# Performance work log

Hardware: AMD Instinct MI355X
Metric: run time of the kernel (lower is better)

The kernel has to match this reference:

```python
import jax, jax.numpy as jnp
import numpy as np

N, E, D, L, G = 100000, 800000, 64, 5, 256
ATOM_VOCAB, BOND_VOCAB = 119, 5
BN_EPS = 1e-5

def _bn(h, g, b):
    # BatchNorm1d in training mode: batch mean / biased var over nodes
    m = h.mean(0)
    v = h.var(0)
    return g * (h - m) * jax.lax.rsqrt(v + BN_EPS) + b

def setup_inputs() -> dict:
    key = jax.random.key(0)
    ks = jax.random.split(key, 12)
    xavier = lambda k, fi, fo: jax.random.uniform(k, (fi, fo), jnp.float32,
                                                  -np.sqrt(6.0/(fi+fo)), np.sqrt(6.0/(fi+fo)))
    return {
        "batch": jnp.sort(jax.random.randint(ks[0], (N,), 0, G)),
        "x": jax.random.randint(ks[1], (N, 1), 0, ATOM_VOCAB),
        "edge_index": jax.random.randint(ks[2], (2, E), 0, N),
        "edge_attr": jax.random.randint(ks[3], (E, 1), 0, BOND_VOCAB),
        "atom_emb": jax.random.normal(ks[4], (ATOM_VOCAB, D), jnp.float32),
        "bond_emb": jax.random.normal(ks[5], (BOND_VOCAB, D), jnp.float32),
        "W1": jnp.stack([xavier(jax.random.fold_in(ks[6], i), D, 2*D) for i in range(L)]),
        "b1": jnp.zeros((L, 2*D), jnp.float32),
        "g1": jnp.ones((L, 2*D), jnp.float32),
        "be1": jnp.zeros((L, 2*D), jnp.float32),
        "W2": jnp.stack([xavier(jax.random.fold_in(ks[7], i), 2*D, D) for i in range(L)]),
        "b2": jnp.zeros((L, D), jnp.float32),
        "gbn": jnp.ones((L, D), jnp.float32),
        "bbn": jnp.zeros((L, D), jnp.float32),
    }

def reference(batch, x, edge_index, edge_attr, atom_emb, bond_emb,
              W1, b1, g1, be1, W2, b2, gbn, bbn):
    h = atom_emb[x[:, 0]]              # [N, D]
    ea = bond_emb[edge_attr[:, 0]]     # [E, D]
    src, dst = edge_index[0], edge_index[1]
    for i in range(L):
        msg = jax.nn.relu(h[src] + ea)                         # [E, D]
        aggr = jax.ops.segment_sum(msg, dst, num_segments=N)   # [N, D]
        z = h + aggr                                           # (1+eps)*x_i + aggr, eps=0
        z = _bn(z @ W1[i] + b1[i], g1[i], be1[i])
        z = jax.nn.relu(z) @ W2[i] + b2[i]
        h = _bn(z, gbn[i], bbn[i])                             # outer BN
        if i < L - 1:
            h = jax.nn.relu(h)                                 # drop_ratio = 0 -> no dropout
    xpool = jax.ops.segment_sum(h, batch, num_segments=G)      # global_add_pool
    return (xpool, h)
```

## Files before the change

### kernel.cpp

```cpp
#include <hip/hip_runtime.h>
#include <cstdint>
#include <cstddef>

#define NN 100000
#define NP 100032
#define NE 800000
#define NG 256
#define NL 5
#define EPS 1e-5f

typedef __bf16 bf16x8 __attribute__((ext_vector_type(8)));
typedef float f32x4 __attribute__((ext_vector_type(4)));

__device__ __forceinline__ float bf2f(unsigned short u) {
  union { unsigned int i; float f; } x; x.i = ((unsigned int)u) << 16; return x.f;
}
__device__ __forceinline__ unsigned short f2bf(float f) {
  union { float f; unsigned int i; } x; x.f = f;
  unsigned int r = x.i + 0x7fffu + ((x.i >> 16) & 1u);
  return (unsigned short)(r >> 16);
}

__global__ __launch_bounds__(256) void init_h_k(const int* __restrict__ x,
                                                const float* __restrict__ atom_emb,
                                                unsigned short* __restrict__ A) {
  int i = blockIdx.x * 256 + threadIdx.x;
  int n = i >> 3, c0 = (i & 7) * 8;
  const float* p = atom_emb + (size_t)x[n] * 64 + c0;
  float4 v0 = *(const float4*)p;
  float4 v1 = *(const float4*)(p + 4);
  union { bf16x8 b; unsigned short u[8]; } o;
  o.u[0] = f2bf(v0.x); o.u[1] = f2bf(v0.y); o.u[2] = f2bf(v0.z); o.u[3] = f2bf(v0.w);
  o.u[4] = f2bf(v1.x); o.u[5] = f2bf(v1.y); o.u[6] = f2bf(v1.z); o.u[7] = f2bf(v1.w);
  *(bf16x8*)(A + (size_t)n * 64 + c0) = o.b;
}

__global__ __launch_bounds__(256) void wconv_k(const float* __restrict__ W1,
                                               const float* __restrict__ W2,
                                               unsigned short* __restrict__ Wt1,
                                               unsigned short* __restrict__ Wt2) {
  int i = blockIdx.x * 256 + threadIdx.x;
  const int S = NL * 128 * 64;
  if (i < S) {
    int l = i / (128 * 64), r = i % (128 * 64);
    int c = r / 64, k = r % 64;
    Wt1[i] = f2bf(W1[(size_t)l * 64 * 128 + (size_t)k * 128 + c]);
  } else if (i < 2 * S) {
    int j = i - S;
    int l = j / (128 * 64), r = j % (128 * 64);
    int c = r / 128, k = r % 128;
    Wt2[j] = f2bf(W2[(size_t)l * 128 * 64 + (size_t)k * 64 + c]);
  }
}

__global__ __launch_bounds__(256) void hist_k(const int* __restrict__ ei,
                                              int* __restrict__ cnt) {
  int e = blockIdx.x * 256 + threadIdx.x;
  if (e >= NE) return;
  atomicAdd(&cnt[ei[NE + e]], 1);
}

__global__ __launch_bounds__(256) void scan1_k(const int* __restrict__ cnt,
                                               int* __restrict__ rs,
                                               int* __restrict__ bsum) {
  __shared__ int sh[256];
  int t = threadIdx.x;
  int base = blockIdx.x * 1024 + t * 4;
  int v0 = 0, v1 = 0, v2 = 0, v3 = 0;
  if (base + 0 < NN) v0 = cnt[base + 0];
  if (base + 1 < NN) v1 = cnt[base + 1];
  if (base + 2 < NN) v2 = cnt[base + 2];
  if (base + 3 < NN) v3 = cnt[base + 3];
  int tsum = v0 + v1 + v2 + v3;
  sh[t] = tsum;
  __syncthreads();
  for (int off = 1; off < 256; off <<= 1) {
    int x = (t >= off) ? sh[t - off] : 0;
    __syncthreads();
    sh[t] += x;
    __syncthreads();
  }
  int excl = sh[t] - tsum;
  if (base + 0 < NN) rs[base + 0] = excl;
  if (base + 1 < NN) rs[base + 1] = excl + v0;
  if (base + 2 < NN) rs[base + 2] = excl + v0 + v1;
  if (base + 3 < NN) rs[base + 3] = excl + v0 + v1 + v2;
  if (t == 255) bsum[blockIdx.x] = sh[255];
}

__global__ void scan2_k(const int* __restrict__ bsum, int* __restrict__ bofs, int nb) {
  if (threadIdx.x == 0 && blockIdx.x == 0) {
    int run = 0;
    for (int i = 0; i < nb; ++i) { bofs[i] = run; run += bsum[i]; }
  }
}

__global__ __launch_bounds__(256) void scan3_k(int* __restrict__ rs,
                                               const int* __restrict__ bofs,
                                               int* __restrict__ cursor) {
  int i = blockIdx.x * 256 + threadIdx.x;
  if (i < NN) {
    int v = rs[i] + bofs[i >> 10];
    rs[i] = v;
    cursor[i] = v;
  }
  if (i == 0) rs[NN] = NE;
}

__global__ __launch_bounds__(256) void scatter_k(const int* __restrict__ ei,
                                                 const int* __restrict__ eattr,
                                                 int* __restrict__ cursor,
                                                 int* __restrict__ epack) {
  int band = blockIdx.x & 7;
  int e = (blockIdx.x >> 3) * 256 + threadIdx.x;
  if (e >= NE) return;
  int d = ei[NE + e];
  if (d / 12500 != band) return;
  int slot = atomicAdd(&cursor[d], 1);
  epack[slot] = (ei[e] << 3) | eattr[e];
}

template <int MODE>
__global__ __launch_bounds__(256) void csr_aggr_k(const int* __restrict__ rowstart,
                                                  const int* __restrict__ epack,
                                                  const float* __restrict__ bond,
                                                  const unsigned short* __restrict__ A,
                                                  const float* __restrict__ stat2prev,
                                                  const float* __restrict__ g,
                                                  const float* __restrict__ be,
                                                  unsigned short* __restrict__ B) {
  __shared__ float bl[5][68];
  __shared__ float scl64[64], shf64[64];
  int tid = threadIdx.x;
  for (int j = tid; j < 320; j += 256) bl[j >> 6][j & 63] = bond[j];
  if (MODE && tid < 64) {
    float s = 0.f, s2 = 0.f;
#pragma unroll
    for (int r = 0; r < 8; ++r) { s += stat2prev[r * 128 + tid]; s2 += stat2prev[r * 128 + 64 + tid]; }
    float mean = s * (1.f / NN);
    float var = fmaxf(s2 * (1.f / NN) - mean * mean, 0.f);
    float sc = g[tid] * rsqrtf(var + EPS);
    scl64[tid] = sc;
    shf64[tid] = be[tid] - mean * sc;
  }
  __syncthreads();

  int w = tid >> 6, lane = tid & 63;
  int es = lane >> 3, cg = lane & 7, c0 = cg * 8;
  float sc[8], sf[8];
  if (MODE) {
#pragma unroll
    for (int j = 0; j < 8; ++j) { sc[j] = scl64[c0 + j]; sf[j] = shf64[c0 + j]; }
  }
  int base16 = blockIdx.x * 16 + w * 4;
#pragma unroll
  for (int r4 = 0; r4 < 4; ++r4) {
    int w0 = base16 + r4;
    int s = rowstart[w0], e = rowstart[w0 + 1];
    float acc[8];
#pragma unroll
    for (int j = 0; j < 8; ++j) acc[j] = 0.f;
    for (int base = s; base < e; base += 64) {
      int m = e - base; if (m > 64) m = 64;
      int pk = (lane < m) ? epack[base + lane] : 0;
      int iters = (m + 7) >> 3;
      for (int i = 0; i < iters; ++i) {
        int idx = i * 8 + es;
        int p = __shfl(pk, idx);
        if (idx < m) {
          union { bf16x8 b; unsigned short u[8]; } hv;
          hv.b = *(const bf16x8*)(A + (size_t)(p >> 3) * 64 + c0);
          const float* bp = &bl[p & 7][c0];
          float4 b0 = *(const float4*)(bp);
          float4 b1 = *(const float4*)(bp + 4);
          float bb[8] = {b0.x, b0.y, b0.z, b0.w, b1.x, b1.y, b1.z, b1.w};
#pragma unroll
          for (int j = 0; j < 8; ++j) {
            float v = bf2f(hv.u[j]);
            if (MODE) v = fmaxf(fmaf(v, sc[j], sf[j]), 0.f);
            acc[j] += fmaxf(v + bb[j], 0.f);
          }
        }
      }
    }
#pragma unroll
    for (int j = 0; j < 8; ++j) {
      acc[j] += __shfl_xor(acc[j], 8);
      acc[j] += __shfl_xor(acc[j], 16);
      acc[j] += __shfl_xor(acc[j], 32);
    }
    if (es == 0) {
      union { bf16x8 b; unsigned short u[8]; } rv, o;
      rv.b = *(const bf16x8*)(A + (size_t)w0 * 64 + c0);
#pragma unroll
      for (int j = 0; j < 8; ++j) {
        float r = bf2f(rv.u[j]);
        if (MODE) r = fmaxf(fmaf(r, sc[j], sf[j]), 0.f);
        o.u[j] = f2bf(acc[j] + r);
      }
      *(bf16x8*)(B + (size_t)w0 * 64 + c0) = o.b;
    }
  }
}

__global__ __launch_bounds__(256) void stat1_k(const unsigned short* __restrict__ B,
                                               const unsigned short* __restrict__ Wt1,
                                               float* __restrict__ stat1) {
  int tid = threadIdx.x;
  int w = tid >> 6, lane = tid & 63;
  int rlo = lane & 15, khi = lane >> 4;
  bf16x8 wf0[8], wf1[8];
#pragma unroll
  for (int ct = 0; ct < 8; ++ct) {
    const bf16x8* bp = (const bf16x8*)(Wt1 + (size_t)(ct * 16 + rlo) * 64 + khi * 8);
    wf0[ct] = bp[0];
    wf1[ct] = bp[4];
  }
  float s[8], s2[8];
#pragma unroll
  for (int ct = 0; ct < 8; ++ct) { s[ct] = 0.f; s2[ct] = 0.f; }
  union { bf16x8 b; uint4 u; } zz; zz.u = make_uint4(0, 0, 0, 0);
  for (int t = blockIdx.x * 4 + w; t < NP / 16; t += 1024) {
    int row = t * 16 + rlo;
    bf16x8 a0, a1;
    if (row < NN) {
      const bf16x8* ap = (const bf16x8*)(B + (size_t)row * 64 + khi * 8);
      a0 = ap[0]; a1 = ap[4];
    } else {
      a0 = zz.b; a1 = zz.b;
    }
#pragma unroll
    for (int ct = 0; ct < 8; ++ct) {
      f32x4 acc;
      acc[0] = 0.f; acc[1] = 0.f; acc[2] = 0.f; acc[3] = 0.f;
      acc = __builtin_amdgcn_mfma_f32_16x16x32_bf16(a0, wf0[ct], acc, 0, 0, 0);
      acc = __builtin_amdgcn_mfma_f32_16x16x32_bf16(a1, wf1[ct], acc, 0, 0, 0);
#pragma unroll
      for (int q = 0; q < 4; ++q) {
        s[ct] += acc[q];
        s2[ct] = fmaf(acc[q], acc[q], s2[ct]);
      }
    }
  }
#pragma unroll
  for (int ct = 0; ct < 8; ++ct) {
    s[ct] += __shfl_xor(s[ct], 16);  s[ct] += __shfl_xor(s[ct], 32);
    s2[ct] += __shfl_xor(s2[ct], 16); s2[ct] += __shfl_xor(s2[ct], 32);
  }
  if (khi == 0) {
    float* dst = stat1 + (blockIdx.x & 7) * 256;
#pragma unroll
    for (int ct = 0; ct < 8; ++ct) {
      atomicAdd(&dst[ct * 16 + rlo], s[ct]);
      atomicAdd(&dst[128 + ct * 16 + rlo], s2[ct]);
    }
  }
}

__global__ __launch_bounds__(256) void gemm12_k(const unsigned short* __restrict__ B,
                                                const unsigned short* __restrict__ Wt1,
                                                const unsigned short* __restrict__ Wt2,
                                                const float* __restrict__ stat1,
                                                const float* __restrict__ g1,
                                                const float* __restrict__ be1,
                                                const float* __restrict__ b2,
                                                unsigned short* __restrict__ z2b,
                                                float* __restrict__ stat2f) {
  __shared__ unsigned short Zs[64][136];
  __shared__ float sclS[128], shfS[128], sred[128];
  int tid = threadIdx.x;
  if (tid < 128) {
    float s = 0.f, s2 = 0.f;
#pragma unroll
    for (int r = 0; r < 8; ++r) { s += stat1[r * 256 + tid]; s2 += stat1[r * 256 + 128 + tid]; }
    float mean = s * (1.f / NN);
    float var = fmaxf(s2 * (1.f / NN) - mean * mean, 0.f);
    float sc = g1[tid] * rsqrtf(var + EPS);
    sclS[tid] = sc;
    shfS[tid] = be1[tid] - mean * sc;
    sred[tid] = 0.f;
  }
  __syncthreads();
  int w = tid >> 6, lane = tid & 63;
  int rlo = lane & 15, khi = lane >> 4;
  int row0 = blockIdx.x * 64 + w * 16;
  const bf16x8* ap = (const bf16x8*)(B + (size_t)(row0 + rlo) * 64 + khi * 8);
  bf16x8 a0 = ap[0], a1 = ap[4];
#pragma unroll
  for (int ct = 0; ct < 8; ++ct) {
    const bf16x8* bp = (const bf16x8*)(Wt1 + (size_t)(ct * 16 + rlo) * 64 + khi * 8);
    f32x4 acc;
    acc[0] = 0.f; acc[1] = 0.f; acc[2] = 0.f; acc[3] = 0.f;
    acc = __builtin_amdgcn_mfma_f32_16x16x32_bf16(a0, bp[0], acc, 0, 0, 0);
    acc = __builtin_amdgcn_mfma_f32_16x16x32_bf16(a1, bp[4], acc, 0, 0, 0);
    int c = ct * 16 + rlo;
    float sc = sclS[c], sf = shfS[c];
#pragma unroll
    for (int q = 0; q < 4; ++q)
      Zs[w * 16 + khi * 4 + q][c] = f2bf(fmaxf(fmaf(acc[q], sc, sf), 0.f));
  }
  bf16x8 af0 = *(const bf16x8*)&Zs[w * 16 + rlo][khi * 8];
  bf16x8 af1 = *(const bf16x8*)&Zs[w * 16 + rlo][32 + khi * 8];
  bf16x8 af2 = *(const bf16x8*)&Zs[w * 16 + rlo][64 + khi * 8];
  bf16x8 af3 = *(const bf16x8*)&Zs[w * 16 + rlo][96 + khi * 8];
  __syncthreads();
  f32x4 acc2[4];
#pragma unroll
  for (int ct = 0; ct < 4; ++ct) { acc2[ct][0] = 0.f; acc2[ct][1] = 0.f; acc2[ct][2] = 0.f; acc2[ct][3] = 0.f; }
#pragma unroll
  for (int ct = 0; ct < 4; ++ct) {
    const bf16x8* bp = (const bf16x8*)(Wt2 + (size_t)(ct * 16 + rlo) * 128 + khi * 8);
    acc2[ct] = __builtin_amdgcn_mfma_f32_16x16x32_bf16(af0, bp[0], acc2[ct], 0, 0, 0);
    acc2[ct] = __builtin_amdgcn_mfma_f32_16x16x32_bf16(af1, bp[4], acc2[ct], 0, 0, 0);
    acc2[ct] = __builtin_amdgcn_mfma_f32_16x16x32_bf16(af2, bp[8], acc2[ct], 0, 0, 0);
    acc2[ct] = __builtin_amdgcn_mfma_f32_16x16x32_bf16(af3, bp[12], acc2[ct], 0, 0, 0);
  }
  unsigned short (*Z2)[72] = (unsigned short(*)[72])Zs;
#pragma unroll
  for (int ct = 0; ct < 4; ++ct) {
    int c = ct * 16 + rlo;
    float bs = b2[c];
    float s = 0.f, s2 = 0.f;
#pragma unroll
    for (int q = 0; q < 4; ++q) {
      int brow = w * 16 + khi * 4 + q;
      float v = acc2[ct][q] + bs;
      unsigned short ub = f2bf(v);
      Z2[brow][c] = ub;
      float vf = bf2f(ub);
      if (blockIdx.x * 64 + brow < NN) { s += vf; s2 += vf * vf; }
    }
    atomicAdd(&sred[c], s);
    atomicAdd(&sred[64 + c], s2);
  }
  __syncthreads();
#pragma unroll
  for (int pass = 0; pass < 2; ++pass) {
    int orow = pass * 32 + (tid >> 3), oc0 = (tid & 7) * 8;
    *(bf16x8*)(z2b + (size_t)(blockIdx.x * 64 + orow) * 64 + oc0) =
        *(const bf16x8*)&Z2[orow][oc0];
  }
  if (tid < 128) atomicAdd(&stat2f[(blockIdx.x & 7) * 128 + tid], sred[tid]);
}

__global__ __launch_bounds__(256) void bn_final_k(const unsigned short* __restrict__ A,
                                                  const float* __restrict__ stat2f,
                                                  const float* __restrict__ g,
                                                  const float* __restrict__ be,
                                                  float* __restrict__ hf) {
  __shared__ float scl[64], shf[64];
  int tid = threadIdx.x;
  if (tid < 64) {
    float s = 0.f, s2 = 0.f;
#pragma unroll
    for (int r = 0; r < 8; ++r) { s += stat2f[r * 128 + tid]; s2 += stat2f[r * 128 + 64 + tid]; }
    float mean = s * (1.f / NN);
    float var = fmaxf(s2 * (1.f / NN) - mean * mean, 0.f);
    float sc = g[tid] * rsqrtf(var + EPS);
    scl[tid] = sc;
    shf[tid] = be[tid] - mean * sc;
  }
  __syncthreads();
  int i = blockIdx.x * 256 + tid;
  int n = i >> 3, c0 = (i & 7) * 8;
  union { bf16x8 b; unsigned short u[8]; } raw;
  raw.b = *(const bf16x8*)(A + (size_t)n * 64 + c0);
  float v[8];
#pragma unroll
  for (int j = 0; j < 8; ++j) v[j] = fmaf(bf2f(raw.u[j]), scl[c0 + j], shf[c0 + j]);
  float* p = hf + (size_t)n * 64 + c0;
  *(float4*)(p)     = make_float4(v[0], v[1], v[2], v[3]);
  *(float4*)(p + 4) = make_float4(v[4], v[5], v[6], v[7]);
}

__global__ __launch_bounds__(256) void pool_k(const float* __restrict__ h,
                                              const int* __restrict__ batch,
                                              float* __restrict__ xpool) {
  int n0 = blockIdx.x * 16;
  int tid = threadIdx.x;
  int r = tid >> 4, c4 = tid & 15;
  int n = n0 + r;
  float4 v = *(const float4*)(h + (size_t)n * 64 + c4 * 4);
  __shared__ int gfirst, gsame;
  __shared__ float red[16][64];
  if (tid == 0) {
    gfirst = batch[n0];
    gsame = (batch[n0] == batch[n0 + 15]) ? 1 : 0;
  }
  *(float4*)&red[r][c4 * 4] = v;
  __syncthreads();
  if (gsame) {
#pragma unroll
    for (int off = 8; off >= 1; off >>= 1) {
      if (r < off) {
        float4 a = *(float4*)&red[r][c4 * 4];
        float4 b = *(float4*)&red[r + off][c4 * 4];
        *(float4*)&red[r][c4 * 4] = make_float4(a.x + b.x, a.y + b.y, a.z + b.z, a.w + b.w);
      }
      __syncthreads();
    }
    if (r == 0) {
      float* p = xpool + (size_t)gfirst * 64 + c4 * 4;
      float4 a = *(float4*)&red[0][c4 * 4];
      atomicAdd(p + 0, a.x); atomicAdd(p + 1, a.y);
      atomicAdd(p + 2, a.z); atomicAdd(p + 3, a.w);
    }
  } else {
    int g = batch[n];
    float* p = xpool + (size_t)g * 64 + c4 * 4;
    atomicAdd(p + 0, v.x); atomicAdd(p + 1, v.y);
    atomicAdd(p + 2, v.z); atomicAdd(p + 3, v.w);
  }
}

extern "C" void kernel_launch(void* const* d_in, const int* in_sizes, int n_in,
                              void* d_out, int out_size, void* d_ws, size_t ws_size,
                              hipStream_t stream) {
  const int* batch = (const int*)d_in[0];
  const int* x = (const int*)d_in[1];
  const int* ei = (const int*)d_in[2];
  const int* eattr = (const int*)d_in[3];
  const float* atom_emb = (const float*)d_in[4];
  const float* bond_emb = (const float*)d_in[5];
  const float* W1 = (const float*)d_in[6];
  const float* g1 = (const float*)d_in[8];
  const float* be1 = (const float*)d_in[9];
  const float* W2 = (const float*)d_in[10];
  const float* b2 = (const float*)d_in[11];
  const float* gbn = (const float*)d_in[12];
  const float* bbn = (const float*)d_in[13];

  float* out = (float*)d_out;
  float* xpool = out;
  float* hf = out + NG * 64;

  char* ws = (char*)d_ws;
  unsigned short* A   = (unsigned short*)(ws);
  unsigned short* B   = (unsigned short*)(ws + 12804096);
  float* sbuf         = (float*)(ws + 25608192);
  unsigned short* Wt1 = (unsigned short*)(ws + 25669632);
  unsigned short* Wt2 = (unsigned short*)(ws + 25751552);
  int* rowstart       = (int*)(ws + 25833472);
  int* epack          = (int*)(ws + 26233600);
  int* cnt    = (int*)(ws + 12804096);
  int* cursor = (int*)(ws + 12804096 + 1048576);
  int* bsum   = (int*)(ws + 12804096 + 2097152);
  int* bofs   = bsum + 128;

  init_h_k<<<NN * 8 / 256, 256, 0, stream>>>(x, atom_emb, A);
  wconv_k<<<(2 * NL * 128 * 64 + 255) / 256, 256, 0, stream>>>(W1, W2, Wt1, Wt2);

  hipMemsetAsync(cnt, 0, (size_t)NN * 4, stream);
  hist_k<<<(NE + 255) / 256, 256, 0, stream>>>(ei, cnt);
  scan1_k<<<98, 256, 0, stream>>>(cnt, rowstart, bsum);
  scan2_k<<<1, 64, 0, stream>>>(bsum, bofs, 98);
  scan3_k<<<(NN + 255) / 256, 256, 0, stream>>>(rowstart, bofs, cursor);
  scatter_k<<<8 * ((NE + 255) / 256), 256, 0, stream>>>(ei, eattr, cursor, epack);

  hipMemsetAsync(sbuf, 0, 61440, stream);
  for (int l = 0; l < NL; ++l) {
    float* stat1 = sbuf + (size_t)l * 3072;
    float* stat2 = sbuf + (size_t)l * 3072 + 2048;
    float* stat2p = sbuf + (size_t)(l - 1) * 3072 + 2048;
    if (l == 0)
      csr_aggr_k<0><<<NN / 16, 256, 0, stream>>>(rowstart, epack, bond_emb, A,
                                                 sbuf, gbn, bbn, B);
    else
      csr_aggr_k<1><<<NN / 16, 256, 0, stream>>>(rowstart, epack, bond_emb, A,
                                                 stat2p, gbn + (size_t)(l - 1) * 64,
                                                 bbn + (size_t)(l - 1) * 64, B);
    stat1_k<<<256, 256, 0, stream>>>(B, Wt1 + (size_t)l * 128 * 64, stat1);
    gemm12_k<<<NP / 64, 256, 0, stream>>>(B, Wt1 + (size_t)l * 128 * 64,
                                          Wt2 + (size_t)l * 64 * 128,
                                          stat1, g1 + (size_t)l * 128, be1 + (size_t)l * 128,
                                          b2 + (size_t)l * 64, A, stat2);
  }

  bn_final_k<<<NN * 8 / 256, 256, 0, stream>>>(A, sbuf + (size_t)(NL - 1) * 3072 + 2048,
                                               gbn + (size_t)(NL - 1) * 64,
                                               bbn + (size_t)(NL - 1) * 64, hf);

  hipMemsetAsync(xpool, 0, (size_t)NG * 64 * 4, stream);
  pool_k<<<NN / 16, 256, 0, stream>>>(hf, batch, xpool);
}
```

Baseline: 600.4 us.

## Merge prep kernels, fold scan2 into scan3, remap CSR aggregation, fuse BN with pooling

Merges the embedding init, the weight conversion and the count zeroing into a single prep kernel. The serial scan2 kernel is dropped, and each scan3 block now sums the block totals it needs itself. The CSR aggregation kernel now gives each 8-lane group one destination row, unrolled two edges at a time, instead of spreading a row's edges across the whole wavefront and reducing with shuffles. The final BN and global add pool are fused so the output is not re-read. Together these aim to cut launch count and memory traffic, but per-row work in aggregation now depends on node degree, which can leave lanes idle.

Measured after the change: 506.6 us. 1.19x faster.

```diff
diff --git a/kernel.cpp b/kernel.cpp
--- a/kernel.cpp
+++ b/kernel.cpp
@@ -21,35 +21,41 @@
   return (unsigned short)(r >> 16);
 }
 
-__global__ __launch_bounds__(256) void init_h_k(const int* __restrict__ x,
-                                                const float* __restrict__ atom_emb,
-                                                unsigned short* __restrict__ A) {
-  int i = blockIdx.x * 256 + threadIdx.x;
-  int n = i >> 3, c0 = (i & 7) * 8;
-  const float* p = atom_emb + (size_t)x[n] * 64 + c0;
-  float4 v0 = *(const float4*)p;
-  float4 v1 = *(const float4*)(p + 4);
-  union { bf16x8 b; unsigned short u[8]; } o;
-  o.u[0] = f2bf(v0.x); o.u[1] = f2bf(v0.y); o.u[2] = f2bf(v0.z); o.u[3] = f2bf(v0.w);
-  o.u[4] = f2bf(v1.x); o.u[5] = f2bf(v1.y); o.u[6] = f2bf(v1.z); o.u[7] = f2bf(v1.w);
-  *(bf16x8*)(A + (size_t)n * 64 + c0) = o.b;
-}
-
-__global__ __launch_bounds__(256) void wconv_k(const float* __restrict__ W1,
-                                               const float* __restrict__ W2,
-                                               unsigned short* __restrict__ Wt1,
-                                               unsigned short* __restrict__ Wt2) {
-  int i = blockIdx.x * 256 + threadIdx.x;
-  const int S = NL * 128 * 64;
-  if (i < S) {
-    int l = i / (128 * 64), r = i % (128 * 64);
-    int c = r / 64, k = r % 64;
-    Wt1[i] = f2bf(W1[(size_t)l * 64 * 128 + (size_t)k * 128 + c]);
-  } else if (i < 2 * S) {
-    int j = i - S;
-    int l = j / (128 * 64), r = j % (128 * 64);
-    int c = r / 128, k = r % 128;
-    Wt2[j] = f2bf(W2[(size_t)l * 128 * 64 + (size_t)k * 64 + c]);
+__global__ __launch_bounds__(256) void prep_k(const int* __restrict__ x,
+                                              const float* __restrict__ atom_emb,
+                                              unsigned short* __restrict__ A,
+                                              const float* __restrict__ W1,
+                                              const float* __restrict__ W2,
+                                              unsigned short* __restrict__ Wt1,
+                                              unsigned short* __restrict__ Wt2,
+                                              int* __restrict__ cnt) {
+  int b = blockIdx.x, t = threadIdx.x;
+  if (b < 3125) {
+    int i = b * 256 + t;
+    int n = i >> 3, c0 = (i & 7) * 8;
+    const float* p = atom_emb + (size_t)x[n] * 64 + c0;
+    float4 v0 = *(const float4*)p;
+    float4 v1 = *(const float4*)(p + 4);
+    union { bf16x8 b8; unsigned short u[8]; } o;
+    o.u[0] = f2bf(v0.x); o.u[1] = f2bf(v0.y); o.u[2] = f2bf(v0.z); o.u[3] = f2bf(v0.w);
+    o.u[4] = f2bf(v1.x); o.u[5] = f2bf(v1.y); o.u[6] = f2bf(v1.z); o.u[7] = f2bf(v1.w);
+    *(bf16x8*)(A + (size_t)n * 64 + c0) = o.b8;
+  } else if (b < 3445) {
+    int i = (b - 3125) * 256 + t;
+    const int S = NL * 128 * 64;
+    if (i < S) {
+      int l = i / (128 * 64), r = i % (128 * 64);
+      int c = r / 64, k = r % 64;
+      Wt1[i] = f2bf(W1[(size_t)l * 64 * 128 + (size_t)k * 128 + c]);
+    } else {
+      int j = i - S;
+      int l = j / (128 * 64), r = j % (128 * 64);
+      int c = r / 128, k = r % 128;
+      Wt2[j] = f2bf(W2[(size_t)l * 128 * 64 + (size_t)k * 64 + c]);
+    }
+  } else {
+    int i = (b - 3445) * 256 + t;
+    if (i < NN) cnt[i] = 0;
   }
 }
 
@@ -88,19 +94,15 @@
   if (t == 255) bsum[blockIdx.x] = sh[255];
 }
 
-__global__ void scan2_k(const int* __restrict__ bsum, int* __restrict__ bofs, int nb) {
-  if (threadIdx.x == 0 && blockIdx.x == 0) {
-    int run = 0;
-    for (int i = 0; i < nb; ++i) { bofs[i] = run; run += bsum[i]; }
-  }
-}
-
 __global__ __launch_bounds__(256) void scan3_k(int* __restrict__ rs,
-                                               const int* __restrict__ bofs,
+                                               const int* __restrict__ bsum,
                                                int* __restrict__ cursor) {
   int i = blockIdx.x * 256 + threadIdx.x;
+  int chunk = blockIdx.x >> 2;
+  int boff = 0;
+  for (int j = 0; j < chunk; ++j) boff += bsum[j];
   if (i < NN) {
-    int v = rs[i] + bofs[i >> 10];
+    int v = rs[i] + boff;
     rs[i] = v;
     cursor[i] = v;
   }
@@ -145,62 +147,65 @@
   }
   __syncthreads();
 
-  int w = tid >> 6, lane = tid & 63;
-  int es = lane >> 3, cg = lane & 7, c0 = cg * 8;
+  int lane = tid & 63;
+  int sg = lane >> 3, ch = lane & 7, c0 = ch * 8;
+  int row = blockIdx.x * 32 + (tid >> 6) * 8 + sg;
   float sc[8], sf[8];
   if (MODE) {
 #pragma unroll
     for (int j = 0; j < 8; ++j) { sc[j] = scl64[c0 + j]; sf[j] = shf64[c0 + j]; }
   }
-  int base16 = blockIdx.x * 16 + w * 4;
-#pragma unroll
-  for (int r4 = 0; r4 < 4; ++r4) {
-    int w0 = base16 + r4;
-    int s = rowstart[w0], e = rowstart[w0 + 1];
-    float acc[8];
-#pragma unroll
-    for (int j = 0; j < 8; ++j) acc[j] = 0.f;
-    for (int base = s; base < e; base += 64) {
-      int m = e - base; if (m > 64) m = 64;
-      int pk = (lane < m) ? epack[base + lane] : 0;
-      int iters = (m + 7) >> 3;
-      for (int i = 0; i < iters; ++i) {
-        int idx = i * 8 + es;
-        int p = __shfl(pk, idx);
-        if (idx < m) {
-          union { bf16x8 b; unsigned short u[8]; } hv;
-          hv.b = *(const bf16x8*)(A + (size_t)(p >> 3) * 64 + c0);
-          const float* bp = &bl[p & 7][c0];
-          float4 b0 = *(const float4*)(bp);
-          float4 b1 = *(const float4*)(bp + 4);
-          float bb[8] = {b0.x, b0.y, b0.z, b0.w, b1.x, b1.y, b1.z, b1.w};
-#pragma unroll
-          for (int j = 0; j < 8; ++j) {
-            float v = bf2f(hv.u[j]);
-            if (MODE) v = fmaxf(fmaf(v, sc[j], sf[j]), 0.f);
-            acc[j] += fmaxf(v + bb[j], 0.f);
-          }
-        }
+  int s = rowstart[row], e = rowstart[row + 1];
+  float acc[8];
+#pragma unroll
+  for (int j = 0; j < 8; ++j) acc[j] = 0.f;
+  int i = s;
+  for (; i + 2 <= e; i += 2) {
+    int p0 = epack[i], p1 = epack[i + 1];
+    union { bf16x8 b; unsigned short u[8]; } h0, h1;
+    h0.b = *(const bf16x8*)(A + (size_t)(p0 >> 3) * 64 + c0);
+    h1.b = *(const bf16x8*)(A + (size_t)(p1 >> 3) * 64 + c0);
+    const float* bp0 = &bl[p0 & 7][c0];
+    const float* bp1 = &bl[p1 & 7][c0];
+    float4 a0 = *(const float4*)(bp0), a1 = *(const float4*)(bp0 + 4);
+    float4 d0 = *(const float4*)(bp1), d1 = *(const float4*)(bp1 + 4);
+    float bb0[8] = {a0.x, a0.y, a0.z, a0.w, a1.x, a1.y, a1.z, a1.w};
+    float bb1[8] = {d0.x, d0.y, d0.z, d0.w, d1.x, d1.y, d1.z, d1.w};
+#pragma unroll
+    for (int j = 0; j < 8; ++j) {
+      float v0 = bf2f(h0.u[j]);
+      float v1 = bf2f(h1.u[j]);
+      if (MODE) {
+        v0 = fmaxf(fmaf(v0, sc[j], sf[j]), 0.f);
+        v1 = fmaxf(fmaf(v1, sc[j], sf[j]), 0.f);
       }
-    }
+      acc[j] += fmaxf(v0 + bb0[j], 0.f);
+      acc[j] += fmaxf(v1 + bb1[j], 0.f);
+    }
+  }
+  if (i < e) {
+    int p0 = epack[i];
+    union { bf16x8 b; unsigned short u[8]; } h0;
+    h0.b = *(const bf16x8*)(A + (size_t)(p0 >> 3) * 64 + c0);
+    const float* bp0 = &bl[p0 & 7][c0];
+    float4 a0 = *(const float4*)(bp0), a1 = *(const float4*)(bp0 + 4);
+    float bb0[8] = {a0.x, a0.y, a0.z, a0.w, a1.x, a1.y, a1.z, a1.w};
 #pragma unroll
     for (int j = 0; j < 8; ++j) {
-      acc[j] += __shfl_xor(acc[j], 8);
-      acc[j] += __shfl_xor(acc[j], 16);
-      acc[j] += __shfl_xor(acc[j], 32);
-    }
-    if (es == 0) {
-      union { bf16x8 b; unsigned short u[8]; } rv, o;
-      rv.b = *(const bf16x8*)(A + (size_t)w0 * 64 + c0);
-#pragma unroll
-      for (int j = 0; j < 8; ++j) {
-        float r = bf2f(rv.u[j]);
-        if (MODE) r = fmaxf(fmaf(r, sc[j], sf[j]), 0.f);
-        o.u[j] = f2bf(acc[j] + r);
-      }
-      *(bf16x8*)(B + (size_t)w0 * 64 + c0) = o.b;
-    }
-  }
+      float v0 = bf2f(h0.u[j]);
+      if (MODE) v0 = fmaxf(fmaf(v0, sc[j], sf[j]), 0.f);
+      acc[j] += fmaxf(v0 + bb0[j], 0.f);
+    }
+  }
+  union { bf16x8 b; unsigned short u[8]; } rv, o;
+  rv.b = *(const bf16x8*)(A + (size_t)row * 64 + c0);
+#pragma unroll
+  for (int j = 0; j < 8; ++j) {
+    float r = bf2f(rv.u[j]);
+    if (MODE) r = fmaxf(fmaf(r, sc[j], sf[j]), 0.f);
+    o.u[j] = f2bf(acc[j] + r);
+  }
+  *(bf16x8*)(B + (size_t)row * 64 + c0) = o.b;
 }
 
 __global__ __launch_bounds__(256) void stat1_k(const unsigned short* __restrict__ B,
@@ -343,12 +348,16 @@
   if (tid < 128) atomicAdd(&stat2f[(blockIdx.x & 7) * 128 + tid], sred[tid]);
 }
 
-__global__ __launch_bounds__(256) void bn_final_k(const unsigned short* __restrict__ A,
-                                                  const float* __restrict__ stat2f,
-                                                  const float* __restrict__ g,
-                                                  const float* __restrict__ be,
-                                                  float* __restrict__ hf) {
+__global__ __launch_bounds__(256) void final_k(const unsigned short* __restrict__ A,
+                                               const float* __restrict__ stat2f,
+                                               const float* __restrict__ g,
+                                               const float* __restrict__ be,
+                                               const int* __restrict__ batch,
+                                               float* __restrict__ hf,
+                                               float* __restrict__ xpool) {
   __shared__ float scl[64], shf[64];
+  __shared__ float red[16][64];
+  __shared__ int gfirst, gsame;
   int tid = threadIdx.x;
   if (tid < 64) {
     float s = 0.f, s2 = 0.f;
@@ -360,54 +369,43 @@
     scl[tid] = sc;
     shf[tid] = be[tid] - mean * sc;
   }
-  __syncthreads();
-  int i = blockIdx.x * 256 + tid;
-  int n = i >> 3, c0 = (i & 7) * 8;
-  union { bf16x8 b; unsigned short u[8]; } raw;
-  raw.b = *(const bf16x8*)(A + (size_t)n * 64 + c0);
-  float v[8];
-#pragma unroll
-  for (int j = 0; j < 8; ++j) v[j] = fmaf(bf2f(raw.u[j]), scl[c0 + j], shf[c0 + j]);
-  float* p = hf + (size_t)n * 64 + c0;
-  *(float4*)(p)     = make_float4(v[0], v[1], v[2], v[3]);
-  *(float4*)(p + 4) = make_float4(v[4], v[5], v[6], v[7]);
-}
-
-__global__ __launch_bounds__(256) void pool_k(const float* __restrict__ h,
-                                              const int* __restrict__ batch,
-                                              float* __restrict__ xpool) {
   int n0 = blockIdx.x * 16;
-  int tid = threadIdx.x;
-  int r = tid >> 4, c4 = tid & 15;
-  int n = n0 + r;
-  float4 v = *(const float4*)(h + (size_t)n * 64 + c4 * 4);
-  __shared__ int gfirst, gsame;
-  __shared__ float red[16][64];
   if (tid == 0) {
     gfirst = batch[n0];
     gsame = (batch[n0] == batch[n0 + 15]) ? 1 : 0;
   }
-  *(float4*)&red[r][c4 * 4] = v;
+  __syncthreads();
+  int r = tid >> 4, c4 = tid & 15;
+  int n = n0 + r;
+  ushort4 raw = *(const ushort4*)(A + (size_t)n * 64 + c4 * 4);
+  int cb = c4 * 4;
+  float4 v;
+  v.x = fmaf(bf2f(raw.x), scl[cb + 0], shf[cb + 0]);
+  v.y = fmaf(bf2f(raw.y), scl[cb + 1], shf[cb + 1]);
+  v.z = fmaf(bf2f(raw.z), scl[cb + 2], shf[cb + 2]);
+  v.w = fmaf(bf2f(raw.w), scl[cb + 3], shf[cb + 3]);
+  *(float4*)(hf + (size_t)n * 64 + cb) = v;
+  *(float4*)&red[r][cb] = v;
   __syncthreads();
   if (gsame) {
 #pragma unroll
     for (int off = 8; off >= 1; off >>= 1) {
       if (r < off) {
-        float4 a = *(float4*)&red[r][c4 * 4];
-        float4 b = *(float4*)&red[r + off][c4 * 4];
-        *(float4*)&red[r][c4 * 4] = make_float4(a.x + b.x, a.y + b.y, a.z + b.z, a.w + b.w);
+        float4 a = *(float4*)&red[r][cb];
+        float4 b = *(float4*)&red[r + off][cb];
+        *(float4*)&red[r][cb] = make_float4(a.x + b.x, a.y + b.y, a.z + b.z, a.w + b.w);
       }
       __syncthreads();
     }
     if (r == 0) {
-      float* p = xpool + (size_t)gfirst * 64 + c4 * 4;
-      float4 a = *(float4*)&red[0][c4 * 4];
+      float* p = xpool + (size_t)gfirst * 64 + cb;
+      float4 a = *(float4*)&red[0][cb];
       atomicAdd(p + 0, a.x); atomicAdd(p + 1, a.y);
       atomicAdd(p + 2, a.z); atomicAdd(p + 3, a.w);
     }
   } else {
-    int g = batch[n];
-    float* p = xpool + (size_t)g * 64 + c4 * 4;
+    int gg = batch[n];
+    float* p = xpool + (size_t)gg * 64 + cb;
     atomicAdd(p + 0, v.x); atomicAdd(p + 1, v.y);
     atomicAdd(p + 2, v.z); atomicAdd(p + 3, v.w);
   }
@@ -445,16 +443,12 @@
   int* cnt    = (int*)(ws + 12804096);
   int* cursor = (int*)(ws + 12804096 + 1048576);
   int* bsum   = (int*)(ws + 12804096 + 2097152);
-  int* bofs   = bsum + 128;
-
-  init_h_k<<<NN * 8 / 256, 256, 0, stream>>>(x, atom_emb, A);
-  wconv_k<<<(2 * NL * 128 * 64 + 255) / 256, 256, 0, stream>>>(W1, W2, Wt1, Wt2);
-
-  hipMemsetAsync(cnt, 0, (size_t)NN * 4, stream);
+
+  prep_k<<<3836, 256, 0, stream>>>(x, atom_emb, A, W1, W2, Wt1, Wt2, cnt);
+
   hist_k<<<(NE + 255) / 256, 256, 0, stream>>>(ei, cnt);
   scan1_k<<<98, 256, 0, stream>>>(cnt, rowstart, bsum);
-  scan2_k<<<1, 64, 0, stream>>>(bsum, bofs, 98);
-  scan3_k<<<(NN + 255) / 256, 256, 0, stream>>>(rowstart, bofs, cursor);
+  scan3_k<<<(NN + 255) / 256, 256, 0, stream>>>(rowstart, bsum, cursor);
   scatter_k<<<8 * ((NE + 255) / 256), 256, 0, stream>>>(ei, eattr, cursor, epack);
 
   hipMemsetAsync(sbuf, 0, 61440, stream);
@@ -463,10 +457,10 @@
     float* stat2 = sbuf + (size_t)l * 3072 + 2048;
     float* stat2p = sbuf + (size_t)(l - 1) * 3072 + 2048;
     if (l == 0)
-      csr_aggr_k<0><<<NN / 16, 256, 0, stream>>>(rowstart, epack, bond_emb, A,
+      csr_aggr_k<0><<<NN / 32, 256, 0, stream>>>(rowstart, epack, bond_emb, A,
                                                  sbuf, gbn, bbn, B);
     else
-      csr_aggr_k<1><<<NN / 16, 256, 0, stream>>>(rowstart, epack, bond_emb, A,
+      csr_aggr_k<1><<<NN / 32, 256, 0, stream>>>(rowstart, epack, bond_emb, A,
                                                  stat2p, gbn + (size_t)(l - 1) * 64,
                                                  bbn + (size_t)(l - 1) * 64, B);
     stat1_k<<<256, 256, 0, stream>>>(B, Wt1 + (size_t)l * 128 * 64, stat1);
@@ -476,10 +470,8 @@
                                           b2 + (size_t)l * 64, A, stat2);
   }
 
-  bn_final_k<<<NN * 8 / 256, 256, 0, stream>>>(A, sbuf + (size_t)(NL - 1) * 3072 + 2048,
-                                               gbn + (size_t)(NL - 1) * 64,
-                                               bbn + (size_t)(NL - 1) * 64, hf);
-
   hipMemsetAsync(xpool, 0, (size_t)NG * 64 * 4, stream);
-  pool_k<<<NN / 16, 256, 0, stream>>>(hf, batch, xpool);
-}
+  final_k<<<NN / 16, 256, 0, stream>>>(A, sbuf + (size_t)(NL - 1) * 3072 + 2048,
+                                       gbn + (size_t)(NL - 1) * 64,
+                                       bbn + (size_t)(NL - 1) * 64, batch, hf, xpool);
+}
```
